# Performance work log

Hardware: AMD Instinct MI355X
Metric: run time of the kernel (lower is better)

## Reference

```python
import jax, jax.numpy as jnp
import numpy as np

H, DK = 8, 32
D_MODEL = H * DK  # 256
Q_DIM = K_DIM = V_DIM = 256
B, T, S = 4, 4, 1024
NEG = -1e10


def setup_inputs() -> dict:
    rng = jax.random.key(0)
    ks = jax.random.split(rng, 12)
    w = lambda k, shp: (jax.random.normal(k, shp, jnp.float32) * 0.02)
    return {
        "query": jax.random.normal(ks[0], (B, T, S, Q_DIM), jnp.float32),
        "key": jax.random.normal(ks[1], (B, T, S, K_DIM), jnp.float32),
        "value": jax.random.normal(ks[2], (B, T, S, V_DIM), jnp.float32),
        "mask": jax.random.randint(ks[3], (B, T), 1, S + 1),  # valid lengths in [1, S]
        "Wq": w(ks[4], (D_MODEL, Q_DIM)), "bq": jnp.zeros((D_MODEL,), jnp.float32),
        "Wk": w(ks[5], (D_MODEL, K_DIM)), "bk": jnp.zeros((D_MODEL,), jnp.float32),
        "Wv": w(ks[6], (D_MODEL, V_DIM)), "bv": jnp.zeros((D_MODEL,), jnp.float32),
        "Wo": w(ks[7], (Q_DIM, D_MODEL)), "bo": jnp.zeros((Q_DIM,), jnp.float32),
    }


def reference(query, key, value, mask, Wq, bq, Wk, bk, Wv, bv, Wo, bo):
    b, t, s, _ = query.shape
    # projections -> [B,T,h,S,d_k]
    def proj(x, W, bias):
        y = jnp.einsum('btsf,df->btsd', x, W) + bias
        return y.reshape(b, t, s, H, DK).transpose(0, 1, 3, 2, 4)
    q = proj(query, Wq, bq)
    k = proj(key, Wk, bk)
    v = proj(value, Wv, bv)
    # scores [B,T,h,S,S]
    scores = jnp.einsum('bthqd,bthkd->bthqk', q, k) / jnp.sqrt(jnp.float32(DK))
    # vectorized length mask: positions < len on both axes (replaces torch python loop)
    valid = jnp.arange(s)[None, None, :] < mask[:, :, None]        # [B,T,S]
    m = valid[:, :, None, :, None] & valid[:, :, None, None, :]    # [B,T,1,S,S]
    scores = jnp.where(m, scores, NEG)
    p = jax.nn.softmax(scores, axis=-1)
    x = jnp.einsum('bthqk,bthkd->bthqd', p, v)                     # [B,T,h,S,d_k]
    x = x.transpose(0, 1, 3, 2, 4).reshape(b, t, s, H * DK)
    return jnp.einsum('btsd,qd->btsq', x, Wo) + bo
```

## Files before the change

kernel.cpp:

```cpp
#include <hip/hip_runtime.h>

#define EXPC 0.25505654442163f

typedef __attribute__((ext_vector_type(8))) short bfrag;
typedef __attribute__((ext_vector_type(4))) float ffrag;
typedef __attribute__((ext_vector_type(8))) unsigned int u8v;
typedef __attribute__((ext_vector_type(4))) unsigned int u4v;
typedef __attribute__((ext_vector_type(2))) unsigned int u2v;

__device__ __forceinline__ short f2bf(float x) {
  union { float f; unsigned u; } v; v.f = x;
  return (short)((v.u + 0x8000u) >> 16);
}

__device__ __forceinline__ unsigned int packbf(float a, float b) {
  return __builtin_amdgcn_perm(__float_as_uint(b) + 0x8000u,
                               __float_as_uint(a) + 0x8000u, 0x07060302u);
}

__device__ __forceinline__ bfrag cvtp(u8v x) {
  u4v r;
#pragma unroll
  for (int i = 0; i < 4; ++i)
    r[i] = __builtin_amdgcn_perm(x[2 * i + 1] + 0x8000u, x[2 * i] + 0x8000u, 0x07060302u);
  union { u4v u; bfrag b; } c; c.u = r; return c.b;
}
__device__ __forceinline__ bfrag cvt8(const float* __restrict__ p) {
  return cvtp(*(const u8v*)p);
}

__global__ __launch_bounds__(256, 3) void proj_kv(
    const float* __restrict__ kin, const float* __restrict__ Wk,
    const float* __restrict__ bk, const float* __restrict__ vin,
    const float* __restrict__ Wv, const float* __restrict__ bv,
    short* __restrict__ ko, short* __restrict__ vt) {
  const int t = threadIdx.x;
  const int lane = t & 63, wid = t >> 6;
  const int lrow = lane & 15, lq = lane >> 4;
  __shared__ __align__(16) char lds[40960];
  short* Ab = (short*)lds;
  short* Bb = (short*)(lds + 20480);
  short* tile = (short*)lds;

  const bool isK = blockIdx.x < 256;
  const int bx = isK ? blockIdx.x : blockIdx.x - 256;
  const int m0 = bx * 64;
  const int row4 = t >> 2, c4 = (t & 3) * 8;

  ffrag acc[4][4] = {};
#pragma unroll 1
  for (int s = 0; s < 8; ++s) {
    const int k0 = s * 32;
    if (s) __syncthreads();
    if (isK) {
      *(bfrag*)(Ab + row4 * 40 + c4) =
          cvt8(kin + (size_t)(m0 + row4) * 256 + k0 + c4);
#pragma unroll
      for (int seg = 0; seg < 4; ++seg)
        *(bfrag*)(Bb + (seg * 64 + row4) * 40 + c4) =
            cvt8(Wk + (size_t)(seg * 64 + row4) * 256 + k0 + c4);
    } else {
      *(bfrag*)(Bb + row4 * 40 + c4) =
          cvt8(vin + (size_t)(m0 + row4) * 256 + k0 + c4);
#pragma unroll
      for (int seg = 0; seg < 4; ++seg)
        *(bfrag*)(Ab + (seg * 64 + row4) * 40 + c4) =
            cvt8(Wv + (size_t)(seg * 64 + row4) * 256 + k0 + c4);
    }
    __syncthreads();
    bfrag a[4], b[4];
    if (isK) {
#pragma unroll
      for (int i = 0; i < 4; ++i)
        a[i] = *(const bfrag*)(Ab + (i * 16 + lrow) * 40 + lq * 8);
#pragma unroll
      for (int j = 0; j < 4; ++j)
        b[j] = *(const bfrag*)(Bb + (wid * 64 + j * 16 + lrow) * 40 + lq * 8);
    } else {
#pragma unroll
      for (int i = 0; i < 4; ++i)
        a[i] = *(const bfrag*)(Ab + (wid * 64 + i * 16 + lrow) * 40 + lq * 8);
#pragma unroll
      for (int j = 0; j < 4; ++j)
        b[j] = *(const bfrag*)(Bb + (j * 16 + lrow) * 40 + lq * 8);
    }
#pragma unroll
    for (int i = 0; i < 4; ++i)
#pragma unroll
      for (int j = 0; j < 4; ++j)
        acc[i][j] = __builtin_amdgcn_mfma_f32_16x16x32_bf16(a[i], b[j], acc[i][j], 0, 0, 0);
  }
  __syncthreads();

  if (isK) {
#pragma unroll
    for (int j = 0; j < 4; ++j) {
      int d = wid * 64 + j * 16 + lrow;
      float bs = bk[d];
#pragma unroll
      for (int i = 0; i < 4; ++i)
#pragma unroll
        for (int r = 0; r < 4; ++r)
          tile[(i * 16 + lq * 4 + r) * 264 + d] = f2bf(acc[i][j][r] + bs);
    }
    __syncthreads();
#pragma unroll
    for (int p = 0; p < 8; ++p) {
      int row = p * 8 + (t >> 5), c = t & 31;
      bfrag v = *(const bfrag*)(tile + row * 264 + c * 8);
      *(bfrag*)(ko + (size_t)(m0 + row) * 256 + c * 8) = v;
    }
  } else {
#pragma unroll
    for (int i = 0; i < 4; ++i)
#pragma unroll
      for (int r = 0; r < 4; ++r) {
        int d = wid * 64 + i * 16 + lq * 4 + r;
        float bs = bv[d];
#pragma unroll
        for (int j = 0; j < 4; ++j)
          tile[d * 72 + j * 16 + lrow] = f2bf(acc[i][j][r] + bs);
      }
    __syncthreads();
    const int bt = m0 >> 10, sl0 = m0 & 1023;
#pragma unroll
    for (int p = 0; p < 8; ++p) {
      int d = p * 32 + (t >> 3), c = t & 7;
      bfrag v = *(const bfrag*)(tile + d * 72 + c * 8);
      *(bfrag*)(vt + (size_t)bt * 262144 + (size_t)d * 1024 + sl0 + c * 8) = v;
    }
  }
}

__global__ __launch_bounds__(512, 4) void attn_fused(
    const float* __restrict__ query, const float* __restrict__ Wq,
    const float* __restrict__ bq, const float* __restrict__ Wo,
    const float* __restrict__ bo, const short* __restrict__ K,
    const short* __restrict__ Vt, const int* __restrict__ mask,
    float* __restrict__ out) {
  const int lane = threadIdx.x & 63, wid = threadIdx.x >> 6;
  const int lrow = lane & 15, lq = lane >> 4;
  const int id = blockIdx.x;
  const int bt = id & 15;
  const int q0 = (id >> 4) * 32;
  const int L = mask[bt];
  const int h = wid;

  __shared__ __align__(16) short qx[32 * 264];
  __shared__ __align__(16) unsigned int ptbuf[8][16 * 36];
  unsigned int* ptg = &ptbuf[wid][0];

  {
    const int n0 = h * 32;
    const float* X = query + ((size_t)bt * 1024 + q0) * 256;
    ffrag acc[2][2] = {};
#pragma unroll
    for (int k0 = 0; k0 < 256; k0 += 32) {
      bfrag a[2], b[2];
#pragma unroll
      for (int i = 0; i < 2; ++i)
        a[i] = cvt8(X + (size_t)(i * 16 + lrow) * 256 + k0 + lq * 8);
#pragma unroll
      for (int j = 0; j < 2; ++j)
        b[j] = cvt8(Wq + (size_t)(n0 + j * 16 + lrow) * 256 + k0 + lq * 8);
#pragma unroll
      for (int i = 0; i < 2; ++i)
#pragma unroll
        for (int j = 0; j < 2; ++j)
          acc[i][j] = __builtin_amdgcn_mfma_f32_16x16x32_bf16(a[i], b[j], acc[i][j], 0, 0, 0);
    }
#pragma unroll
    for (int j = 0; j < 2; ++j) {
      int d = n0 + j * 16 + lrow;
      float bs = bq[d];
#pragma unroll
      for (int i = 0; i < 2; ++i)
#pragma unroll
        for (int r = 0; r < 4; ++r)
          qx[(i * 16 + lq * 4 + r) * 264 + d] = f2bf((acc[i][j][r] + bs) * EXPC);
    }
  }

  const short* Kb = K + (size_t)bt * 262144;
  const short* Vb = Vt + ((size_t)bt * 8 + h) * 32768;
  bfrag qf[2];
#pragma unroll
  for (int g = 0; g < 2; ++g)
    qf[g] = *(const bfrag*)(qx + (g * 16 + lrow) * 264 + h * 32 + lq * 8);

  const int nvalid = min(max(L - q0, 0), 32);
  const int nchunk = (nvalid > 0) ? ((L + 63) >> 6) : 0;

  float l_loc[2] = {0.f, 0.f};
  ffrag o[2][2] = {};

#pragma unroll 1
  for (int c = 0; c < nchunk; ++c) {
    const int kc = c * 64;
    const ffrag zf = {0.f, 0.f, 0.f, 0.f};
    bfrag kf[4];
#pragma unroll
    for (int f = 0; f < 4; ++f)
      kf[f] = *(const bfrag*)(Kb + (size_t)(kc + f * 16 + lrow) * 256 + h * 32 + lq * 8);
    bfrag av[2][2];
#pragma unroll
    for (int dj = 0; dj < 2; ++dj)
#pragma unroll
      for (int b = 0; b < 2; ++b)
        av[dj][b] = *(const bfrag*)(Vb + (size_t)(dj * 16 + lrow) * 1024 + kc + b * 32 + lq * 8);

    ffrag st[2][4];
#pragma unroll
    for (int g = 0; g < 2; ++g)
#pragma unroll
      for (int f = 0; f < 4; ++f)
        st[g][f] = __builtin_amdgcn_mfma_f32_16x16x32_bf16(kf[f], qf[g], zf, 0, 0, 0);

    const bool fullc = (kc + 64 <= L);
#pragma unroll
    for (int g = 0; g < 2; ++g) {
      float p[4][4];
      if (fullc) {
#pragma unroll
        for (int f = 0; f < 4; ++f)
#pragma unroll
          for (int r = 0; r < 4; ++r) {
            p[f][r] = __builtin_amdgcn_exp2f(st[g][f][r]);
            l_loc[g] += p[f][r];
          }
      } else {
#pragma unroll
        for (int f = 0; f < 4; ++f)
#pragma unroll
          for (int r = 0; r < 4; ++r) {
            int kr = kc + f * 16 + lq * 4 + r;
            float pv = (kr < L) ? __builtin_amdgcn_exp2f(st[g][f][r]) : 0.f;
            p[f][r] = pv;
            l_loc[g] += pv;
          }
      }
#pragma unroll
      for (int f = 0; f < 4; ++f) {
        u2v w;
        w[0] = packbf(p[f][0], p[f][1]);
        w[1] = packbf(p[f][2], p[f][3]);
        *(u2v*)(ptg + lrow * 36 + 8 * f + 2 * lq) = w;
      }
#pragma unroll
      for (int b = 0; b < 2; ++b) {
        u4v pv = *(const u4v*)(ptg + lrow * 36 + 16 * b + 4 * lq);
        union { u4v u; bfrag bf; } pt; pt.u = pv;
#pragma unroll
        for (int dj = 0; dj < 2; ++dj)
          o[g][dj] = __builtin_amdgcn_mfma_f32_16x16x32_bf16(av[dj][b], pt.bf, o[g][dj], 0, 0, 0);
      }
    }
  }

  float l_i[2];
#pragma unroll
  for (int g = 0; g < 2; ++g) {
    float rs = l_loc[g];
    rs += __shfl_xor(rs, 16);
    rs += __shfl_xor(rs, 32);
    l_i[g] = rs;
  }

  if (nvalid < 32) {
#pragma unroll
    for (int g = 0; g < 2; ++g) {
      bool inv = (g * 16 + lrow) >= nvalid;
      if (inv) {
        l_i[g] = 1024.f;
#pragma unroll
        for (int dj = 0; dj < 2; ++dj)
#pragma unroll
          for (int r = 0; r < 4; ++r) o[g][dj][r] = 0.f;
      }
    }
    bfrag ind[2];
#pragma unroll
    for (int g = 0; g < 2; ++g) {
      short iv = ((g * 16 + lrow) >= nvalid) ? (short)0x3F80 : (short)0;
#pragma unroll
      for (int j = 0; j < 8; ++j) ind[g][j] = iv;
    }
    const bool g0 = (nvalid < 16);
#pragma unroll 2
    for (int kc = 0; kc < 1024; kc += 64) {
#pragma unroll
      for (int dj = 0; dj < 2; ++dj)
#pragma unroll
        for (int b = 0; b < 2; ++b) {
          bfrag av = *(const bfrag*)(Vb + (size_t)(dj * 16 + lrow) * 1024 + kc + b * 32 + lq * 8);
          if (g0)
            o[0][dj] = __builtin_amdgcn_mfma_f32_16x16x32_bf16(av, ind[0], o[0][dj], 0, 0, 0);
          o[1][dj] = __builtin_amdgcn_mfma_f32_16x16x32_bf16(av, ind[1], o[1][dj], 0, 0, 0);
        }
    }
  }

#pragma unroll
  for (int g = 0; g < 2; ++g) {
    float rcp = 1.0f / l_i[g];
#pragma unroll
    for (int dj = 0; dj < 2; ++dj) {
      u2v w;
      w[0] = packbf(o[g][dj][0] * rcp, o[g][dj][1] * rcp);
      w[1] = packbf(o[g][dj][2] * rcp, o[g][dj][3] * rcp);
      short* dst = qx + (g * 16 + lrow) * 264 + h * 32 + dj * 16 + lq * 4;
      *(u2v*)dst = w;
    }
  }
  __syncthreads();

  {
    const int n0 = h * 32;
    ffrag acc[2][2] = {};
#pragma unroll
    for (int k0 = 0; k0 < 256; k0 += 32) {
      bfrag a[2], b[2];
#pragma unroll
      for (int i = 0; i < 2; ++i)
        a[i] = *(const bfrag*)(qx + (i * 16 + lrow) * 264 + k0 + lq * 8);
#pragma unroll
      for (int j = 0; j < 2; ++j)
        b[j] = cvt8(Wo + (size_t)(n0 + j * 16 + lrow) * 256 + k0 + lq * 8);
#pragma unroll
      for (int i = 0; i < 2; ++i)
#pragma unroll
        for (int j = 0; j < 2; ++j)
          acc[i][j] = __builtin_amdgcn_mfma_f32_16x16x32_bf16(a[i], b[j], acc[i][j], 0, 0, 0);
    }
#pragma unroll
    for (int j = 0; j < 2; ++j) {
      int d = n0 + j * 16 + lrow;
      float bs = bo[d];
#pragma unroll
      for (int i = 0; i < 2; ++i)
#pragma unroll
        for (int r = 0; r < 4; ++r)
          out[((size_t)bt * 1024 + q0 + i * 16 + lq * 4 + r) * 256 + d] = acc[i][j][r] + bs;
    }
  }
}

extern "C" void kernel_launch(void* const* d_in, const int* in_sizes, int n_in,
                              void* d_out, int out_size, void* d_ws, size_t ws_size,
                              hipStream_t stream) {
  const float* query = (const float*)d_in[0];
  const float* key   = (const float*)d_in[1];
  const float* value = (const float*)d_in[2];
  const int*   mask  = (const int*)d_in[3];
  const float* Wq = (const float*)d_in[4];
  const float* bq = (const float*)d_in[5];
  const float* Wk = (const float*)d_in[6];
  const float* bk = (const float*)d_in[7];
  const float* Wv = (const float*)d_in[8];
  const float* bv = (const float*)d_in[9];
  const float* Wo = (const float*)d_in[10];
  const float* bo = (const float*)d_in[11];
  float* out = (float*)d_out;

  short* k_ws  = (short*)d_ws;
  short* vt_ws = k_ws + 4194304;

  proj_kv<<<dim3(512), 256, 0, stream>>>(key, Wk, bk, value, Wv, bv, k_ws, vt_ws);
  attn_fused<<<dim3(512), 512, 0, stream>>>(query, Wq, bq, Wo, bo,
                                            k_ws, vt_ws, mask, out);
}
```

Measured before the change: 222.8 us.

## Split K/V projection by output half and software-pipeline global loads

The K/V projection kernel now splits each 64-row tile into two 128-column halves, doubling the grid, shrinking LDS to allow more resident blocks, and prefetching the next k-slice into registers while the current slice runs MFMA. The attention kernel register-prefetches the next Q/Wq/Wo slices and the next K chunk, overlapping global latency with compute. It also permutes block-to-batch mapping so neighbouring blocks spread across different masked lengths for load balance. The costs are more register pressure and twice the redundant input-row reads in proj_kv.

```diff
diff --git a/kernel.cpp b/kernel.cpp
--- a/kernel.cpp
+++ b/kernel.cpp
@@ -29,7 +29,7 @@
   return cvtp(*(const u8v*)p);
 }
 
-__global__ __launch_bounds__(256, 3) void proj_kv(
+__global__ __launch_bounds__(256, 4) void proj_kv(
     const float* __restrict__ kin, const float* __restrict__ Wk,
     const float* __restrict__ bk, const float* __restrict__ vin,
     const float* __restrict__ Wv, const float* __restrict__ bv,
@@ -37,97 +37,133 @@
   const int t = threadIdx.x;
   const int lane = t & 63, wid = t >> 6;
   const int lrow = lane & 15, lq = lane >> 4;
-  __shared__ __align__(16) char lds[40960];
-  short* Ab = (short*)lds;
-  short* Bb = (short*)(lds + 20480);
-  short* tile = (short*)lds;
-
-  const bool isK = blockIdx.x < 256;
-  const int bx = isK ? blockIdx.x : blockIdx.x - 256;
-  const int m0 = bx * 64;
+  __shared__ __align__(16) char lds[18432];
   const int row4 = t >> 2, c4 = (t & 3) * 8;
 
-  ffrag acc[4][4] = {};
+  const bool isK = blockIdx.x < 512;
+  if (isK) {
+    const int bx = blockIdx.x >> 1, d0 = (blockIdx.x & 1) * 128;
+    const int m0 = bx * 64;
+    short* Ab = (short*)lds;
+    short* Bb = (short*)(lds + 5120);
+    short* tile = (short*)lds;
+    ffrag acc[4][2] = {};
+    u8v pa, pb0, pb1;
+    pa  = *(const u8v*)(kin + (size_t)(m0 + row4) * 256 + c4);
+    pb0 = *(const u8v*)(Wk + (size_t)(d0 + row4) * 256 + c4);
+    pb1 = *(const u8v*)(Wk + (size_t)(d0 + 64 + row4) * 256 + c4);
+    *(bfrag*)(Ab + row4 * 40 + c4) = cvtp(pa);
+    *(bfrag*)(Bb + row4 * 40 + c4) = cvtp(pb0);
+    *(bfrag*)(Bb + (64 + row4) * 40 + c4) = cvtp(pb1);
 #pragma unroll 1
-  for (int s = 0; s < 8; ++s) {
-    const int k0 = s * 32;
-    if (s) __syncthreads();
-    if (isK) {
-      *(bfrag*)(Ab + row4 * 40 + c4) =
-          cvt8(kin + (size_t)(m0 + row4) * 256 + k0 + c4);
-#pragma unroll
-      for (int seg = 0; seg < 4; ++seg)
-        *(bfrag*)(Bb + (seg * 64 + row4) * 40 + c4) =
-            cvt8(Wk + (size_t)(seg * 64 + row4) * 256 + k0 + c4);
-    } else {
-      *(bfrag*)(Bb + row4 * 40 + c4) =
-          cvt8(vin + (size_t)(m0 + row4) * 256 + k0 + c4);
-#pragma unroll
-      for (int seg = 0; seg < 4; ++seg)
-        *(bfrag*)(Ab + (seg * 64 + row4) * 40 + c4) =
-            cvt8(Wv + (size_t)(seg * 64 + row4) * 256 + k0 + c4);
-    }
-    __syncthreads();
-    bfrag a[4], b[4];
-    if (isK) {
+    for (int s = 0; s < 8; ++s) {
+      __syncthreads();
+      if (s < 7) {
+        const int k1 = (s + 1) * 32;
+        pa  = *(const u8v*)(kin + (size_t)(m0 + row4) * 256 + k1 + c4);
+        pb0 = *(const u8v*)(Wk + (size_t)(d0 + row4) * 256 + k1 + c4);
+        pb1 = *(const u8v*)(Wk + (size_t)(d0 + 64 + row4) * 256 + k1 + c4);
+      }
+      bfrag a[4], b[2];
 #pragma unroll
       for (int i = 0; i < 4; ++i)
         a[i] = *(const bfrag*)(Ab + (i * 16 + lrow) * 40 + lq * 8);
 #pragma unroll
+      for (int j = 0; j < 2; ++j)
+        b[j] = *(const bfrag*)(Bb + (wid * 32 + j * 16 + lrow) * 40 + lq * 8);
+#pragma unroll
+      for (int i = 0; i < 4; ++i)
+#pragma unroll
+        for (int j = 0; j < 2; ++j)
+          acc[i][j] = __builtin_amdgcn_mfma_f32_16x16x32_bf16(a[i], b[j], acc[i][j], 0, 0, 0);
+      __syncthreads();
+      if (s < 7) {
+        *(bfrag*)(Ab + row4 * 40 + c4) = cvtp(pa);
+        *(bfrag*)(Bb + row4 * 40 + c4) = cvtp(pb0);
+        *(bfrag*)(Bb + (64 + row4) * 40 + c4) = cvtp(pb1);
+      }
+    }
+    __syncthreads();
+#pragma unroll
+    for (int j = 0; j < 2; ++j) {
+      int dl = wid * 32 + j * 16 + lrow;
+      float bs = bk[d0 + dl];
+#pragma unroll
+      for (int i = 0; i < 4; ++i)
+#pragma unroll
+        for (int r = 0; r < 4; ++r)
+          tile[(i * 16 + lq * 4 + r) * 136 + dl] = f2bf(acc[i][j][r] + bs);
+    }
+    __syncthreads();
+#pragma unroll
+    for (int p = 0; p < 4; ++p) {
+      int id2 = p * 256 + t;
+      int row = id2 >> 4, c = id2 & 15;
+      bfrag v = *(const bfrag*)(tile + row * 136 + c * 8);
+      *(bfrag*)(ko + (size_t)(m0 + row) * 256 + d0 + c * 8) = v;
+    }
+  } else {
+    const int t2 = blockIdx.x - 512;
+    const int bx = t2 >> 1, d0 = (t2 & 1) * 128;
+    const int n0 = bx * 64;
+    short* Aw = (short*)lds;
+    short* Bv = (short*)(lds + 10240);
+    short* tile = (short*)lds;
+    ffrag acc[2][4] = {};
+    u8v pv, pw0, pw1;
+    pw0 = *(const u8v*)(Wv + (size_t)(d0 + row4) * 256 + c4);
+    pw1 = *(const u8v*)(Wv + (size_t)(d0 + 64 + row4) * 256 + c4);
+    pv  = *(const u8v*)(vin + (size_t)(n0 + row4) * 256 + c4);
+    *(bfrag*)(Aw + row4 * 40 + c4) = cvtp(pw0);
+    *(bfrag*)(Aw + (64 + row4) * 40 + c4) = cvtp(pw1);
+    *(bfrag*)(Bv + row4 * 40 + c4) = cvtp(pv);
+#pragma unroll 1
+    for (int s = 0; s < 8; ++s) {
+      __syncthreads();
+      if (s < 7) {
+        const int k1 = (s + 1) * 32;
+        pw0 = *(const u8v*)(Wv + (size_t)(d0 + row4) * 256 + k1 + c4);
+        pw1 = *(const u8v*)(Wv + (size_t)(d0 + 64 + row4) * 256 + k1 + c4);
+        pv  = *(const u8v*)(vin + (size_t)(n0 + row4) * 256 + k1 + c4);
+      }
+      bfrag a[2], b[4];
+#pragma unroll
+      for (int i = 0; i < 2; ++i)
+        a[i] = *(const bfrag*)(Aw + (wid * 32 + i * 16 + lrow) * 40 + lq * 8);
+#pragma unroll
       for (int j = 0; j < 4; ++j)
-        b[j] = *(const bfrag*)(Bb + (wid * 64 + j * 16 + lrow) * 40 + lq * 8);
-    } else {
-#pragma unroll
-      for (int i = 0; i < 4; ++i)
-        a[i] = *(const bfrag*)(Ab + (wid * 64 + i * 16 + lrow) * 40 + lq * 8);
-#pragma unroll
-      for (int j = 0; j < 4; ++j)
-        b[j] = *(const bfrag*)(Bb + (j * 16 + lrow) * 40 + lq * 8);
-    }
-#pragma unroll
-    for (int i = 0; i < 4; ++i)
-#pragma unroll
-      for (int j = 0; j < 4; ++j)
-        acc[i][j] = __builtin_amdgcn_mfma_f32_16x16x32_bf16(a[i], b[j], acc[i][j], 0, 0, 0);
-  }
-  __syncthreads();
-
-  if (isK) {
-#pragma unroll
-    for (int j = 0; j < 4; ++j) {
-      int d = wid * 64 + j * 16 + lrow;
-      float bs = bk[d];
-#pragma unroll
-      for (int i = 0; i < 4; ++i)
-#pragma unroll
-        for (int r = 0; r < 4; ++r)
-          tile[(i * 16 + lq * 4 + r) * 264 + d] = f2bf(acc[i][j][r] + bs);
+        b[j] = *(const bfrag*)(Bv + (j * 16 + lrow) * 40 + lq * 8);
+#pragma unroll
+      for (int i = 0; i < 2; ++i)
+#pragma unroll
+        for (int j = 0; j < 4; ++j)
+          acc[i][j] = __builtin_amdgcn_mfma_f32_16x16x32_bf16(a[i], b[j], acc[i][j], 0, 0, 0);
+      __syncthreads();
+      if (s < 7) {
+        *(bfrag*)(Aw + row4 * 40 + c4) = cvtp(pw0);
+        *(bfrag*)(Aw + (64 + row4) * 40 + c4) = cvtp(pw1);
+        *(bfrag*)(Bv + row4 * 40 + c4) = cvtp(pv);
+      }
     }
     __syncthreads();
 #pragma unroll
-    for (int p = 0; p < 8; ++p) {
-      int row = p * 8 + (t >> 5), c = t & 31;
-      bfrag v = *(const bfrag*)(tile + row * 264 + c * 8);
-      *(bfrag*)(ko + (size_t)(m0 + row) * 256 + c * 8) = v;
-    }
-  } else {
-#pragma unroll
-    for (int i = 0; i < 4; ++i)
+    for (int i = 0; i < 2; ++i)
 #pragma unroll
       for (int r = 0; r < 4; ++r) {
-        int d = wid * 64 + i * 16 + lq * 4 + r;
-        float bs = bv[d];
+        int dl = wid * 32 + i * 16 + lq * 4 + r;
+        float bs = bv[d0 + dl];
 #pragma unroll
         for (int j = 0; j < 4; ++j)
-          tile[d * 72 + j * 16 + lrow] = f2bf(acc[i][j][r] + bs);
+          tile[dl * 72 + j * 16 + lrow] = f2bf(acc[i][j][r] + bs);
       }
     __syncthreads();
-    const int bt = m0 >> 10, sl0 = m0 & 1023;
-#pragma unroll
-    for (int p = 0; p < 8; ++p) {
-      int d = p * 32 + (t >> 3), c = t & 7;
-      bfrag v = *(const bfrag*)(tile + d * 72 + c * 8);
-      *(bfrag*)(vt + (size_t)bt * 262144 + (size_t)d * 1024 + sl0 + c * 8) = v;
+    const int bt = n0 >> 10, sl0 = n0 & 1023;
+#pragma unroll
+    for (int p = 0; p < 4; ++p) {
+      int id2 = p * 256 + t;
+      int dl = id2 >> 3, c = id2 & 7;
+      bfrag v = *(const bfrag*)(tile + dl * 72 + c * 8);
+      *(bfrag*)(vt + (size_t)bt * 262144 + (size_t)(d0 + dl) * 1024 + sl0 + c * 8) = v;
     }
   }
 }
@@ -141,7 +177,7 @@
   const int lane = threadIdx.x & 63, wid = threadIdx.x >> 6;
   const int lrow = lane & 15, lq = lane >> 4;
   const int id = blockIdx.x;
-  const int bt = id & 15;
+  const int bt = (id + (id >> 8)) & 15;
   const int q0 = (id >> 4) * 32;
   const int L = mask[bt];
   const int h = wid;
@@ -154,20 +190,38 @@
     const int n0 = h * 32;
     const float* X = query + ((size_t)bt * 1024 + q0) * 256;
     ffrag acc[2][2] = {};
-#pragma unroll
-    for (int k0 = 0; k0 < 256; k0 += 32) {
+    u8v xa[2], wb[2], xa_n[2], wb_n[2];
+#pragma unroll
+    for (int i = 0; i < 2; ++i)
+      xa[i] = *(const u8v*)(X + (size_t)(i * 16 + lrow) * 256 + lq * 8);
+#pragma unroll
+    for (int j = 0; j < 2; ++j)
+      wb[j] = *(const u8v*)(Wq + (size_t)(n0 + j * 16 + lrow) * 256 + lq * 8);
+#pragma unroll 1
+    for (int tt = 0; tt < 8; ++tt) {
+      if (tt < 7) {
+        const int kk = (tt + 1) * 32;
+#pragma unroll
+        for (int i = 0; i < 2; ++i)
+          xa_n[i] = *(const u8v*)(X + (size_t)(i * 16 + lrow) * 256 + kk + lq * 8);
+#pragma unroll
+        for (int j = 0; j < 2; ++j)
+          wb_n[j] = *(const u8v*)(Wq + (size_t)(n0 + j * 16 + lrow) * 256 + kk + lq * 8);
+      }
       bfrag a[2], b[2];
 #pragma unroll
-      for (int i = 0; i < 2; ++i)
-        a[i] = cvt8(X + (size_t)(i * 16 + lrow) * 256 + k0 + lq * 8);
-#pragma unroll
-      for (int j = 0; j < 2; ++j)
-        b[j] = cvt8(Wq + (size_t)(n0 + j * 16 + lrow) * 256 + k0 + lq * 8);
+      for (int i = 0; i < 2; ++i) a[i] = cvtp(xa[i]);
+#pragma unroll
+      for (int j = 0; j < 2; ++j) b[j] = cvtp(wb[j]);
 #pragma unroll
       for (int i = 0; i < 2; ++i)
 #pragma unroll
         for (int j = 0; j < 2; ++j)
           acc[i][j] = __builtin_amdgcn_mfma_f32_16x16x32_bf16(a[i], b[j], acc[i][j], 0, 0, 0);
+#pragma unroll
+      for (int i = 0; i < 2; ++i) xa[i] = xa_n[i];
+#pragma unroll
+      for (int j = 0; j < 2; ++j) wb[j] = wb_n[j];
     }
 #pragma unroll
     for (int j = 0; j < 2; ++j) {
@@ -193,15 +247,23 @@
 
   float l_loc[2] = {0.f, 0.f};
   ffrag o[2][2] = {};
+
+  bfrag kf[4], kf_n[4];
+  if (nchunk > 0) {
+#pragma unroll
+    for (int f = 0; f < 4; ++f)
+      kf[f] = *(const bfrag*)(Kb + (size_t)(f * 16 + lrow) * 256 + h * 32 + lq * 8);
+  }
 
 #pragma unroll 1
   for (int c = 0; c < nchunk; ++c) {
     const int kc = c * 64;
     const ffrag zf = {0.f, 0.f, 0.f, 0.f};
-    bfrag kf[4];
-#pragma unroll
-    for (int f = 0; f < 4; ++f)
-      kf[f] = *(const bfrag*)(Kb + (size_t)(kc + f * 16 + lrow) * 256 + h * 32 + lq * 8);
+    if (c + 1 < nchunk) {
+#pragma unroll
+      for (int f = 0; f < 4; ++f)
+        kf_n[f] = *(const bfrag*)(Kb + (size_t)(kc + 64 + f * 16 + lrow) * 256 + h * 32 + lq * 8);
+    }
     bfrag av[2][2];
 #pragma unroll
     for (int dj = 0; dj < 2; ++dj)
@@ -255,6 +317,8 @@
           o[g][dj] = __builtin_amdgcn_mfma_f32_16x16x32_bf16(av[dj][b], pt.bf, o[g][dj], 0, 0, 0);
       }
     }
+#pragma unroll
+    for (int f = 0; f < 4; ++f) kf[f] = kf_n[f];
   }
 
   float l_i[2];
@@ -317,20 +381,31 @@
   {
     const int n0 = h * 32;
     ffrag acc[2][2] = {};
-#pragma unroll
-    for (int k0 = 0; k0 < 256; k0 += 32) {
+    u8v wb[2], wb_n[2];
+#pragma unroll
+    for (int j = 0; j < 2; ++j)
+      wb[j] = *(const u8v*)(Wo + (size_t)(n0 + j * 16 + lrow) * 256 + lq * 8);
+#pragma unroll 1
+    for (int tt = 0; tt < 8; ++tt) {
+      const int k0 = tt * 32;
+      if (tt < 7) {
+#pragma unroll
+        for (int j = 0; j < 2; ++j)
+          wb_n[j] = *(const u8v*)(Wo + (size_t)(n0 + j * 16 + lrow) * 256 + k0 + 32 + lq * 8);
+      }
       bfrag a[2], b[2];
 #pragma unroll
       for (int i = 0; i < 2; ++i)
         a[i] = *(const bfrag*)(qx + (i * 16 + lrow) * 264 + k0 + lq * 8);
 #pragma unroll
-      for (int j = 0; j < 2; ++j)
-        b[j] = cvt8(Wo + (size_t)(n0 + j * 16 + lrow) * 256 + k0 + lq * 8);
+      for (int j = 0; j < 2; ++j) b[j] = cvtp(wb[j]);
 #pragma unroll
       for (int i = 0; i < 2; ++i)
 #pragma unroll
         for (int j = 0; j < 2; ++j)
           acc[i][j] = __builtin_amdgcn_mfma_f32_16x16x32_bf16(a[i], b[j], acc[i][j], 0, 0, 0);
+#pragma unroll
+      for (int j = 0; j < 2; ++j) wb[j] = wb_n[j];
     }
 #pragma unroll
     for (int j = 0; j < 2; ++j) {
@@ -365,7 +440,7 @@
   short* k_ws  = (short*)d_ws;
   short* vt_ws = k_ws + 4194304;
 
-  proj_kv<<<dim3(512), 256, 0, stream>>>(key, Wk, bk, value, Wv, bv, k_ws, vt_ws);
+  proj_kv<<<dim3(1024), 256, 0, stream>>>(key, Wk, bk, value, Wv, bv, k_ws, vt_ws);
   attn_fused<<<dim3(512), 512, 0, stream>>>(query, Wq, bq, Wo, bo,
                                             k_ws, vt_ws, mask, out);
 }
```

Result: faster. 218.1 us (-2.1%).
